# Kernel tuning notes

Measured on AMD Instinct MI355X. Metric: run time of the kernel, lower is better.

Reference implementation:

```python
import jax, jax.numpy as jnp
import numpy as np

T, S, B, H, NH, F = 256, 128, 32, 1024, 16, 4096
D = H // NH  # head dim


def setup_inputs() -> dict:
    key = jax.random.key(0)
    ks = jax.random.split(key, 14)
    w = lambda k, shape: jax.random.normal(k, shape, jnp.float32) * 0.02
    return {
        "x": jax.random.normal(ks[0], (T, B, H), jnp.float32),
        "src_bias": jnp.zeros((B, 1, 1, S), jnp.float32),
        "tgt_bias": jnp.zeros((B, 1, 1, T), jnp.float32),
        "memory": jax.random.normal(ks[1], (S, B, H), jnp.float32),
        # cross-attention projections
        "Wq": w(ks[2], (H, H)), "bq": jnp.zeros((H,), jnp.float32),
        "Wk": w(ks[3], (H, H)), "bk": jnp.zeros((H,), jnp.float32),
        "Wv": w(ks[4], (H, H)), "bv": jnp.zeros((H,), jnp.float32),
        "Wo": w(ks[5], (H, H)), "bo": jnp.zeros((H,), jnp.float32),
        # feed-forward
        "W1": w(ks[6], (H, F)), "b1": jnp.zeros((F,), jnp.float32),
        "W2": w(ks[7], (F, H)), "b2": jnp.zeros((H,), jnp.float32),
        # LSTM gates: input = cat(ffn_x, attn_ctx, h) -> 3H, output 4H (i,j,f,o)
        "Wg": w(ks[8], (3 * H, 4 * H)), "bg": jnp.zeros((4 * H,), jnp.float32),
    }


def _cross_attention(xq, mem, bias, Wq, bq, Wk, bk, Wv, bv, Wo, bo):
    # xq: [B,T,H], mem: [B,S,H], bias: [B,1,1,S]
    b, t, h = xq.shape
    q = (xq @ Wq + bq).reshape(b, t, NH, D) * (D ** -0.5)
    k = (mem @ Wk + bk).reshape(b, -1, NH, D)
    v = (mem @ Wv + bv).reshape(b, -1, NH, D)
    logits = jnp.einsum("bqhd,bkhd->bhqk", q, k) + bias
    wts = jax.nn.softmax(logits, axis=-1)
    ctx = jnp.einsum("bhqk,bkhd->bqhd", wts, v).reshape(b, t, h)
    return ctx @ Wo + bo


def reference(x, src_bias, tgt_bias, memory, Wq, bq, Wk, bk, Wv, bv, Wo, bo,
              W1, b1, W2, b2, Wg, bg):
    # cross attention (time-major -> batch-major -> time-major)
    c_attn = _cross_attention(jnp.transpose(x, (1, 0, 2)),
                              jnp.transpose(memory, (1, 0, 2)),
                              src_bias, Wq, bq, Wk, bk, Wv, bv, Wo, bo)
    c_attn = jnp.transpose(c_attn, (1, 0, 2))  # [T,B,H]

    # feed-forward on x (dropout disabled / eval mode)
    ffn_x = jax.nn.relu(x @ W1 + b1) @ W2 + b2  # [T,B,H]

    xs = jnp.concatenate([ffn_x, c_attn], axis=-1)  # [T,B,2H]
    c0 = jnp.zeros((x.shape[1], H), x.dtype)
    h0 = jnp.zeros((x.shape[1], H), x.dtype)

    def step(carry, xt):
        c, h = carry
        g = jnp.concatenate([xt, h], axis=-1) @ Wg + bg  # [B,4H]
        i = jax.nn.sigmoid(g[:, :H])
        j = jnp.tanh(g[:, H:2 * H])
        f = jax.nn.sigmoid(g[:, 2 * H:3 * H])
        o = jax.nn.sigmoid(g[:, 3 * H:])
        new_c = f * c + i * j
        new_h = o * new_c  # THUMT LSTMCell default activation=None
        return (new_c, new_h), new_h

    (c_f, h_f), hiddens = jax.lax.scan(step, (c0, h0), xs)
    return hiddens, c_f, h_f
```

## Files before the change

### kernel.cpp

```cpp
#include <hip/hip_runtime.h>
#include <cstdint>
#include <cstddef>

#define T_  256
#define S_  128
#define B_  32
#define H_  1024
#define NH_ 16
#define D_  64
#define F_  4096
#define TB_ (T_*B_)
#define SB_ (S_*B_)

typedef unsigned short u16;
typedef unsigned int   u32;
typedef unsigned long long u64;
typedef __attribute__((ext_vector_type(8))) short s16x8;
typedef __attribute__((ext_vector_type(4))) float f32x4;
typedef __attribute__((ext_vector_type(4))) u32  u32x4;

static __device__ __forceinline__ float b2f(u16 u) {
  union { u32 i; float f; } cv; cv.i = ((u32)u) << 16; return cv.f;
}
static __device__ __forceinline__ u16 f2b(float f) {
  union { float f; u32 i; } cv; cv.f = f;
  u32 u = cv.i;
  u32 r = (u + 0x7fffu + ((u >> 16) & 1u)) >> 16;
  return (u16)r;
}
static __device__ __forceinline__ float sigm(float x) {
  return 1.0f / (1.0f + __expf(-x));
}
static __device__ __forceinline__ float tanh_fast(float x) {
  float e2 = __expf(2.0f * x);
  return 1.0f - 2.0f / (e2 + 1.0f);
}

typedef const __attribute__((address_space(1))) void* gvoidp;
typedef __attribute__((address_space(3))) void* lvoidp;
static __device__ __forceinline__ void gl_lds16(const void* g, void* l) {
  __builtin_amdgcn_global_load_lds((gvoidp)g, (lvoidp)l, 16, 0, 0);
}

static __device__ __forceinline__ void cast_task(const float* __restrict__ in,
                                                 u16* __restrict__ out, int lb, int tid) {
  int i = lb * 256 + tid;
  float4 v = reinterpret_cast<const float4*>(in)[i];
  ushort4 o;
  o.x = f2b(v.x); o.y = f2b(v.y); o.z = f2b(v.z); o.w = f2b(v.w);
  reinterpret_cast<ushort4*>(out)[i] = o;
}

static __device__ __forceinline__ void tr32(const float* __restrict__ in,
                                            u16* __restrict__ out,
                                            int R, int C, int lin, int tid,
                                            float tile[32][33]) {
  const int gx = C >> 5;
  const int bx = lin % gx, by = lin / gx;
  const int c0 = bx << 5, r0 = by << 5;
  const int tx = tid & 31, ty = tid >> 5;
  #pragma unroll
  for (int k = 0; k < 32; k += 8)
    tile[ty + k][tx] = in[(size_t)(r0 + ty + k) * C + c0 + tx];
  __syncthreads();
  #pragma unroll
  for (int k = 0; k < 32; k += 8)
    out[(size_t)(c0 + ty + k) * R + r0 + tx] = f2b(tile[tx][ty + k]);
}

#define NB_SENT 1
#define NB_CX   8192
#define NB_CM   4096
#define NB_TSQ  1024
#define NB_TW1  4096
#define NB_TW2  4096
#define NB_TGX  8192
#define NB_TWH  4096
#define NB_PREP (NB_SENT + NB_CX + NB_CM + 4*NB_TSQ + NB_TW1 + NB_TW2 + NB_TGX + NB_TWH)

__global__ __launch_bounds__(256) void prep_all(
    const float* __restrict__ x, const float* __restrict__ mem,
    const float* __restrict__ Wq, const float* __restrict__ Wk,
    const float* __restrict__ Wv, const float* __restrict__ Wo,
    const float* __restrict__ W1, const float* __restrict__ W2,
    const float* __restrict__ Wg,
    u16* __restrict__ xb, u16* __restrict__ memb,
    u16* __restrict__ WqT, u16* __restrict__ WkT, u16* __restrict__ WvT,
    u16* __restrict__ WoT, u16* __restrict__ W1T, u16* __restrict__ W2T,
    u16* __restrict__ WgxT, u16* __restrict__ WhT, u32* __restrict__ sent)
{
  __shared__ float tile[32][33];
  int b = blockIdx.x;
  const int tid = threadIdx.x;
  if (b < NB_SENT) { sent[tid] = 0; sent[tid + 256] = 0; return; }
  b -= NB_SENT;
  if (b < NB_CX) { cast_task(x, xb, b, tid); return; }      b -= NB_CX;
  if (b < NB_CM) { cast_task(mem, memb, b, tid); return; }  b -= NB_CM;
  if (b < NB_TSQ) { tr32(Wq, WqT, H_, H_, b, tid, tile); return; }  b -= NB_TSQ;
  if (b < NB_TSQ) { tr32(Wk, WkT, H_, H_, b, tid, tile); return; }  b -= NB_TSQ;
  if (b < NB_TSQ) { tr32(Wv, WvT, H_, H_, b, tid, tile); return; }  b -= NB_TSQ;
  if (b < NB_TSQ) { tr32(Wo, WoT, H_, H_, b, tid, tile); return; }  b -= NB_TSQ;
  if (b < NB_TW1) { tr32(W1, W1T, H_, F_, b, tid, tile); return; }  b -= NB_TW1;
  if (b < NB_TW2) { tr32(W2, W2T, F_, H_, b, tid, tile); return; }  b -= NB_TW2;
  if (b < NB_TGX) { tr32(Wg, WgxT, 2 * H_, 4 * H_, b, tid, tile); return; } b -= NB_TGX;
  tr32(Wg + (size_t)(2 * H_) * (4 * H_), WhT, H_, 4 * H_, b, tid, tile);
}

static __device__ __forceinline__ void gemm_core(
    const u16* __restrict__ A, const u16* __restrict__ Bt,
    u16* __restrict__ Out, const float* __restrict__ bias,
    int Kdim, int ostride, float scale, int relu,
    int bx, int by, u16* As, u16* Bs)
{
  const int tid  = threadIdx.x;
  const int wave = tid >> 6, lane = tid & 63;
  const int quad = lane >> 4, l16 = lane & 15;
  const int bm = by << 7, bn = bx << 7;
  const int wm = (wave & 1) << 6, wn = (wave >> 1) << 6;
  f32x4 acc[4][4] = {};

  const int sr = wave * 32 + (lane >> 2);
  const int sc = (lane & 3) * 8;
  const u16* ga = &A [(size_t)(bm + sr) * Kdim + sc];
  const u16* gb = &Bt[(size_t)(bn + sr) * Kdim + sc];
  u16* lA = &As[wave * 1024];
  u16* lB = &Bs[wave * 1024];
  const size_t rowskip = (size_t)16 * Kdim;

  for (int k0 = 0; k0 < Kdim; k0 += 32) {
    gl_lds16(ga + k0,           lA);
    gl_lds16(ga + k0 + rowskip, lA + 512);
    gl_lds16(gb + k0,           lB);
    gl_lds16(gb + k0 + rowskip, lB + 512);
    __syncthreads();
    s16x8 af[4], bf[4];
    #pragma unroll
    for (int mt = 0; mt < 4; mt++)
      af[mt] = *(const s16x8*)&As[(wm + mt * 16 + l16) * 32 + quad * 8];
    #pragma unroll
    for (int nt = 0; nt < 4; nt++)
      bf[nt] = *(const s16x8*)&Bs[(wn + nt * 16 + l16) * 32 + quad * 8];
    #pragma unroll
    for (int mt = 0; mt < 4; mt++)
      #pragma unroll
      for (int nt = 0; nt < 4; nt++)
        acc[mt][nt] = __builtin_amdgcn_mfma_f32_16x16x32_bf16(af[mt], bf[nt], acc[mt][nt], 0, 0, 0);
    __syncthreads();
  }

  #pragma unroll
  for (int mt = 0; mt < 4; mt++) {
    #pragma unroll
    for (int nt = 0; nt < 4; nt++) {
      const int col = bn + wn + nt * 16 + l16;
      const float bv = bias[col];
      #pragma unroll
      for (int r = 0; r < 4; r++) {
        const int row = bm + wm + mt * 16 + quad * 4 + r;
        float vv = (acc[mt][nt][r] + bv) * scale;
        if (relu) vv = fmaxf(vv, 0.0f);
        Out[(size_t)row * ostride + col] = f2b(vv);
      }
    }
  }
}

struct GJob {
  const u16* A; const u16* Bt; u16* Out; const float* bias;
  int Kdim; int ostride; int relu; int gridx; int nblk; float scale;
};
struct GBatch { GJob j[4]; int starts[4]; int njobs; };

__global__ __launch_bounds__(256) void gemm_multi(GBatch gb)
{
  __shared__ __align__(16) u16 As[128 * 32];
  __shared__ __align__(16) u16 Bs[128 * 32];
  const int bid = blockIdx.x;
  int ji = 0;
  #pragma unroll
  for (int t = 1; t < 4; t++)
    if (t < gb.njobs && bid >= gb.starts[t]) ji = t;
  const GJob J = gb.j[ji];
  const int lin = bid - gb.starts[ji];
  const int wg = (lin & 7) * (J.nblk >> 3) + (lin >> 3);
  const int bx = wg % J.gridx, by = wg / J.gridx;
  gemm_core(J.A, J.Bt, J.Out, J.bias, J.Kdim, J.ostride, J.scale, J.relu, bx, by, As, Bs);
}

__global__ __launch_bounds__(256) void attn_kernel(
    const u16* __restrict__ q, const u16* __restrict__ k, const u16* __restrict__ v,
    const float* __restrict__ src_bias, u16* __restrict__ ctx)
{
  __shared__ u16 ks[S_ * D_];
  __shared__ u16 vs[S_ * D_];
  const int b  = blockIdx.x >> 4;
  const int nh = blockIdx.x & 15;
  const int tid = threadIdx.x;

  for (int i = tid; i < (S_ * D_) / 8; i += 256) {
    int s = i >> 3, c = (i & 7) * 8;
    *(uint4*)&ks[s * D_ + c] = *(const uint4*)&k[((size_t)(s * B_ + b)) * H_ + nh * D_ + c];
    *(uint4*)&vs[s * D_ + c] = *(const uint4*)&v[((size_t)(s * B_ + b)) * H_ + nh * D_ + c];
  }
  __syncthreads();

  const int t = tid;
  float qf[D_];
  const u16* qp = &q[((size_t)(t * B_ + b)) * H_ + nh * D_];
  #pragma unroll
  for (int c8 = 0; c8 < D_; c8 += 8) {
    uint4 qv = *(const uint4*)&qp[c8];
    const u16* pu = (const u16*)&qv;
    #pragma unroll
    for (int j = 0; j < 8; j++) qf[c8 + j] = b2f(pu[j]);
  }
  const float* bias = src_bias + b * S_;

  float m = -1e30f, l = 0.0f;
  for (int s = 0; s < S_; s++) {
    float dot = 0.0f;
    #pragma unroll
    for (int d = 0; d < D_; d++) dot += qf[d] * b2f(ks[s * D_ + d]);
    dot += bias[s];
    float nm = fmaxf(m, dot);
    l = l * __expf(m - nm) + __expf(dot - nm);
    m = nm;
  }
  float of[D_] = {};
  const float inv = 1.0f / l;
  for (int s = 0; s < S_; s++) {
    float dot = 0.0f;
    #pragma unroll
    for (int d = 0; d < D_; d++) dot += qf[d] * b2f(ks[s * D_ + d]);
    dot += bias[s];
    float w = __expf(dot - m) * inv;
    #pragma unroll
    for (int d = 0; d < D_; d++) of[d] += w * b2f(vs[s * D_ + d]);
  }
  u16* op = &ctx[((size_t)(t * B_ + b)) * H_ + nh * D_];
  #pragma unroll
  for (int c8 = 0; c8 < D_; c8 += 8) {
    u16 tmp[8];
    #pragma unroll
    for (int j = 0; j < 8; j++) tmp[j] = f2b(of[c8 + j]);
    *(uint4*)&op[c8] = *(const uint4*)tmp;
  }
}

#define ISSUE2(K) { \
  const u16* b0_ = hb + ((size_t)(wave * 16 + (K) * 2 + (quad >> 1))) * 512 + \
                   (quad & 1) * 8 + l16 * 16; \
  asm volatile("global_load_dwordx4 %0, %1, off sc0 sc1" : "=v"(ba[K][0]) : "v"(b0_) : "memory"); \
  asm volatile("global_load_dwordx4 %0, %1, off sc0 sc1" : "=v"(ba[K][1]) : "v"(b0_ + 256) : "memory"); }

#define DO_MFMA(A0,A1,KC)                                                           \
  { _Pragma("unroll") for (int g_ = 0; g_ < 3; g_++) {                              \
      s16x8 wf_ = *(const s16x8*)&Wl[wave][((g_ * 8 + (KC)) * 64 + lane) * 8];      \
      acc[g_][0] = __builtin_amdgcn_mfma_f32_16x16x32_bf16(A0, wf_, acc[g_][0], 0, 0, 0); \
      acc[g_][1] = __builtin_amdgcn_mfma_f32_16x16x32_bf16(A1, wf_, acc[g_][1], 0, 0, 0); } \
    acc[3][0] = __builtin_amdgcn_mfma_f32_16x16x32_bf16(A0, wo[KC], acc[3][0], 0, 0, 0);  \
    acc[3][1] = __builtin_amdgcn_mfma_f32_16x16x32_bf16(A1, wo[KC], acc[3][1], 0, 0, 0); }

#define CONSUME(K, NSTR) { \
  asm volatile("s_waitcnt vmcnt(" NSTR ")" ::: "memory"); \
  __builtin_amdgcn_sched_barrier(0); \
  DO_MFMA(ba[K][0], ba[K][1], K); }

__global__ __launch_bounds__(256, 1) void lstm_persistent(
    const u16* __restrict__ g_x, const u16* __restrict__ WhT,
    u16* __restrict__ hb16, u32* __restrict__ sent, float* __restrict__ out)
{
  __shared__ __align__(16) u16 Wl[4][3 * 8 * 64 * 8];
  __shared__ float P[4][4][32][17];
  const int bk = blockIdx.x, tid = threadIdx.x;
  const int wave = tid >> 6, lane = tid & 63;
  const int quad = lane >> 4, l16 = lane & 15;

  for (int i = lane; i < 3 * 8 * 64; i += 64) {
    const int g  = (i >> 9) & 3;
    const int kc = (i >> 6) & 7;
    const int row = g * H_ + bk * 16 + (lane & 15);
    const int col = wave * 256 + kc * 32 + (lane >> 4) * 8;
    *(uint4*)&Wl[wave][i * 8] = *(const uint4*)&WhT[(size_t)row * H_ + col];
  }
  s16x8 wo[8];
  {
    const int row = 3 * H_ + bk * 16 + (lane & 15);
    const int colb = wave * 256 + (lane >> 4) * 8;
    #pragma unroll
    for (int kc = 0; kc < 8; kc++)
      wo[kc] = *(const s16x8*)&WhT[(size_t)row * H_ + colb + kc * 32];
  }
  __syncthreads();

  const int pb = tid >> 4, pc = tid & 15;
  const int col = bk * 16 + pc;
  float creg[2] = {0.0f, 0.0f};

  float gxp[2][4];
  #pragma unroll
  for (int ii = 0; ii < 2; ii++)
    #pragma unroll
    for (int g = 0; g < 4; g++)
      gxp[ii][g] = b2f(g_x[((size_t)(pb + ii * 16)) * (4 * H_) + g * H_ + col]);

  s16x8 ba[8][2];

  for (int t = 0; t < T_; t++) {
    if (t > 0) {
      const u32 st = (u32)t;
      const u16* hb = hb16 + ((t & 1) ^ 1) * 32768;

      { const u32* sp = sent + ((size_t)(((t & 1) ^ 1) * 256 + wave * 64 + lane));
        u32 sv;
        do {
          asm volatile("global_load_dword %0, %1, off sc0 sc1\n\ts_waitcnt vmcnt(0)"
                       : "=v"(sv) : "v"(sp) : "memory");
        } while (!__all(sv == st)); }

      f32x4 acc[4][2] = {};
      ISSUE2(0) ISSUE2(1) ISSUE2(2) ISSUE2(3)
      ISSUE2(4) ISSUE2(5) ISSUE2(6) ISSUE2(7)
      CONSUME(0, "14") CONSUME(1, "12") CONSUME(2, "10") CONSUME(3, "8")
      CONSUME(4, "6")  CONSUME(5, "4")  CONSUME(6, "2")  CONSUME(7, "0")

      #pragma unroll
      for (int g = 0; g < 4; g++)
        #pragma unroll
        for (int mt = 0; mt < 2; mt++)
          #pragma unroll
          for (int r = 0; r < 4; r++)
            P[wave][g][mt * 16 + quad * 4 + r][l16] = acc[g][mt][r];
    }
    __syncthreads();

    float gs[2][4];
    #pragma unroll
    for (int ii = 0; ii < 2; ii++) {
      const int b_ = pb + ii * 16;
      #pragma unroll
      for (int g = 0; g < 4; g++) {
        float s = gxp[ii][g];
        if (t > 0) s += P[0][g][b_][pc] + P[1][g][b_][pc] + P[2][g][b_][pc] + P[3][g][b_][pc];
        gs[ii][g] = s;
      }
    }
    __syncthreads();

    float hn[2], cn[2];
    #pragma unroll
    for (int ii = 0; ii < 2; ii++) {
      const float iv = sigm(gs[ii][0]);
      const float jv = tanh_fast(gs[ii][1]);
      const float fv = sigm(gs[ii][2]);
      const float ov = sigm(gs[ii][3]);
      cn[ii] = fv * creg[ii] + iv * jv;
      hn[ii] = ov * cn[ii];
      creg[ii] = cn[ii];
    }

    {
      u32 lo0 = f2b(hn[0]), lo1 = f2b(hn[1]);
      u32 hi0 = __shfl_down(lo0, 1), hi1 = __shfl_down(lo1, 1);
      if ((pc & 1) == 0) {
        u32* hw32 = (u32*)(hb16 + (t & 1) * 32768);
        u32 dw0 = lo0 | (hi0 << 16);
        u32 dw1 = lo1 | (hi1 << 16);
        __hip_atomic_store(&hw32[(size_t)bk * 256 + pb * 8 + (pc >> 1)], dw0,
                           __ATOMIC_RELAXED, __HIP_MEMORY_SCOPE_AGENT);
        __hip_atomic_store(&hw32[(size_t)bk * 256 + (pb + 16) * 8 + (pc >> 1)], dw1,
                           __ATOMIC_RELAXED, __HIP_MEMORY_SCOPE_AGENT);
      }
      asm volatile("s_waitcnt vmcnt(0)" ::: "memory");
      if (lane == 0)
        __hip_atomic_store(&sent[(size_t)(t & 1) * 256 + bk * 4 + wave], (u32)(t + 1),
                           __ATOMIC_RELAXED, __HIP_MEMORY_SCOPE_AGENT);
    }

    #pragma unroll
    for (int ii = 0; ii < 2; ii++) {
      const int b_ = pb + ii * 16;
      out[(size_t)t * (B_ * H_) + b_ * H_ + col] = hn[ii];
      if (t == T_ - 1) {
        out[(size_t)T_ * B_ * H_ + b_ * H_ + col] = cn[ii];
        out[(size_t)T_ * B_ * H_ + B_ * H_ + b_ * H_ + col] = hn[ii];
      }
    }
    if (t < T_ - 1) {
      #pragma unroll
      for (int ii = 0; ii < 2; ii++)
        #pragma unroll
        for (int g = 0; g < 4; g++)
          gxp[ii][g] = b2f(g_x[((size_t)(t + 1) * B_ + pb + ii * 16) * (4 * H_) + g * H_ + col]);
    }
  }
}

extern "C" void kernel_launch(void* const* d_in, const int* in_sizes, int n_in,
                              void* d_out, int out_size, void* d_ws, size_t ws_size,
                              hipStream_t stream)
{
  const float* x        = (const float*)d_in[0];
  const float* src_bias = (const float*)d_in[1];
  const float* mem      = (const float*)d_in[3];
  const float* Wq = (const float*)d_in[4];  const float* bq = (const float*)d_in[5];
  const float* Wk = (const float*)d_in[6];  const float* bk = (const float*)d_in[7];
  const float* Wv = (const float*)d_in[8];  const float* bv = (const float*)d_in[9];
  const float* Wo = (const float*)d_in[10]; const float* bo = (const float*)d_in[11];
  const float* W1 = (const float*)d_in[12]; const float* b1f = (const float*)d_in[13];
  const float* W2 = (const float*)d_in[14]; const float* b2f_ = (const float*)d_in[15];
  const float* Wg = (const float*)d_in[16]; const float* bg = (const float*)d_in[17];
  float* out = (float*)d_out;

  char* p = (char*)d_ws;
  u16* xb   = (u16*)p; p += (size_t)TB_ * H_ * 2;
  u16* memb = (u16*)p; p += (size_t)SB_ * H_ * 2;
  u16* WqT  = (u16*)p; p += (size_t)H_ * H_ * 2;
  u16* WkT  = (u16*)p; p += (size_t)H_ * H_ * 2;
  u16* WvT  = (u16*)p; p += (size_t)H_ * H_ * 2;
  u16* WoT  = (u16*)p; p += (size_t)H_ * H_ * 2;
  u16* W1T  = (u16*)p; p += (size_t)F_ * H_ * 2;
  u16* W2T  = (u16*)p; p += (size_t)H_ * F_ * 2;
  u16* WgxT = (u16*)p; p += (size_t)(4 * H_) * (2 * H_) * 2;
  u16* WhT  = (u16*)p; p += (size_t)(4 * H_) * H_ * 2;
  u16* qb   = (u16*)p; p += (size_t)TB_ * H_ * 2;
  u16* kb   = (u16*)p; p += (size_t)SB_ * H_ * 2;
  u16* vb   = (u16*)p; p += (size_t)SB_ * H_ * 2;
  u16* ctxb = (u16*)p; p += (size_t)TB_ * H_ * 2;
  u16* xs   = (u16*)p; p += (size_t)TB_ * (2 * H_) * 2;
  u16* h1   = (u16*)p; p += (size_t)TB_ * F_ * 2;
  u16* hb16 = (u16*)p; p += (size_t)2 * 32768 * 2;
  u32* sent = (u32*)p; p += (size_t)2 * 256 * 4;
  u16* gx   = h1;

  prep_all<<<dim3(NB_PREP), dim3(256), 0, stream>>>(
      x, mem, Wq, Wk, Wv, Wo, W1, W2, Wg,
      xb, memb, WqT, WkT, WvT, WoT, W1T, W2T, WgxT, WhT, sent);

  GBatch gb1 = {};
  gb1.j[0] = { xb,   WqT, qb, bq,  H_,     H_,     0,  H_ / 128,     TB_ / 128 * (H_ / 128),      0.125f };
  gb1.j[1] = { memb, WkT, kb, bk,  H_,     H_,     0,  H_ / 128,     SB_ / 128 * (H_ / 128),      1.0f   };
  gb1.j[2] = { memb, WvT, vb, bv,  H_,     H_,     0,  H_ / 128,     SB_ / 128 * (H_ / 128),      1.0f   };
  gb1.j[3] = { xb,   W1T, h1, b1f, H_,     F_,     1,  F_ / 128,     TB_ / 128 * (F_ / 128),      1.0f   };
  gb1.starts[0] = 0;
  gb1.starts[1] = gb1.j[0].nblk;
  gb1.starts[2] = gb1.starts[1] + gb1.j[1].nblk;
  gb1.starts[3] = gb1.starts[2] + gb1.j[2].nblk;
  gb1.njobs = 4;
  const int nb1 = gb1.starts[3] + gb1.j[3].nblk;
  gemm_multi<<<dim3(nb1), dim3(256), 0, stream>>>(gb1);

  attn_kernel<<<dim3(B_ * NH_), dim3(256), 0, stream>>>(qb, kb, vb, src_bias, ctxb);

  GBatch gb2 = {};
  gb2.j[0] = { ctxb, WoT, xs + H_, bo,   H_, 2 * H_, 0, H_ / 128, TB_ / 128 * (H_ / 128), 1.0f };
  gb2.j[1] = { h1,   W2T, xs,      b2f_, F_, 2 * H_, 0, H_ / 128, TB_ / 128 * (H_ / 128), 1.0f };
  gb2.starts[0] = 0;
  gb2.starts[1] = gb2.j[0].nblk;
  gb2.njobs = 2;
  const int nb2 = gb2.starts[1] + gb2.j[1].nblk;
  gemm_multi<<<dim3(nb2), dim3(256), 0, stream>>>(gb2);

  GBatch gb3 = {};
  gb3.j[0] = { xs, WgxT, gx, bg, 2 * H_, 4 * H_, 0, 4 * H_ / 128, TB_ / 128 * (4 * H_ / 128), 1.0f };
  gb3.starts[0] = 0;
  gb3.njobs = 1;
  gemm_multi<<<dim3(gb3.j[0].nblk), dim3(256), 0, stream>>>(gb3);

  lstm_persistent<<<dim3(64), dim3(256), 0, stream>>>(gx, WhT, hb16, sent, out);
}
```

Before: 1.697 ms.

## Replace 128x128 GEMM with double-buffered 256x256 tile pipelined kernel

Replaces the 128x128-tile, 4-wave, single-buffered GEMM with a 256x256-tile, 8-wave kernel. It stages the next K-tile into a second LDS buffer while MFMAs run, using manual vmcnt waits, s_barrier and setprio, and XOR-swizzles LDS rows to avoid bank conflicts. The larger tiles raise data reuse per block and the overlap hides global load latency. The cost is fewer blocks per GEMM, which can under-fill the GPU for the small K/V projections, plus 128KB of LDS per block and heavier register use.

```diff
diff --git a/kernel.cpp b/kernel.cpp
--- a/kernel.cpp
+++ b/kernel.cpp
@@ -106,64 +106,9 @@
   tr32(Wg + (size_t)(2 * H_) * (4 * H_), WhT, H_, 4 * H_, b, tid, tile);
 }
 
-static __device__ __forceinline__ void gemm_core(
-    const u16* __restrict__ A, const u16* __restrict__ Bt,
-    u16* __restrict__ Out, const float* __restrict__ bias,
-    int Kdim, int ostride, float scale, int relu,
-    int bx, int by, u16* As, u16* Bs)
-{
-  const int tid  = threadIdx.x;
-  const int wave = tid >> 6, lane = tid & 63;
-  const int quad = lane >> 4, l16 = lane & 15;
-  const int bm = by << 7, bn = bx << 7;
-  const int wm = (wave & 1) << 6, wn = (wave >> 1) << 6;
-  f32x4 acc[4][4] = {};
-
-  const int sr = wave * 32 + (lane >> 2);
-  const int sc = (lane & 3) * 8;
-  const u16* ga = &A [(size_t)(bm + sr) * Kdim + sc];
-  const u16* gb = &Bt[(size_t)(bn + sr) * Kdim + sc];
-  u16* lA = &As[wave * 1024];
-  u16* lB = &Bs[wave * 1024];
-  const size_t rowskip = (size_t)16 * Kdim;
-
-  for (int k0 = 0; k0 < Kdim; k0 += 32) {
-    gl_lds16(ga + k0,           lA);
-    gl_lds16(ga + k0 + rowskip, lA + 512);
-    gl_lds16(gb + k0,           lB);
-    gl_lds16(gb + k0 + rowskip, lB + 512);
-    __syncthreads();
-    s16x8 af[4], bf[4];
-    #pragma unroll
-    for (int mt = 0; mt < 4; mt++)
-      af[mt] = *(const s16x8*)&As[(wm + mt * 16 + l16) * 32 + quad * 8];
-    #pragma unroll
-    for (int nt = 0; nt < 4; nt++)
-      bf[nt] = *(const s16x8*)&Bs[(wn + nt * 16 + l16) * 32 + quad * 8];
-    #pragma unroll
-    for (int mt = 0; mt < 4; mt++)
-      #pragma unroll
-      for (int nt = 0; nt < 4; nt++)
-        acc[mt][nt] = __builtin_amdgcn_mfma_f32_16x16x32_bf16(af[mt], bf[nt], acc[mt][nt], 0, 0, 0);
-    __syncthreads();
-  }
-
-  #pragma unroll
-  for (int mt = 0; mt < 4; mt++) {
-    #pragma unroll
-    for (int nt = 0; nt < 4; nt++) {
-      const int col = bn + wn + nt * 16 + l16;
-      const float bv = bias[col];
-      #pragma unroll
-      for (int r = 0; r < 4; r++) {
-        const int row = bm + wm + mt * 16 + quad * 4 + r;
-        float vv = (acc[mt][nt][r] + bv) * scale;
-        if (relu) vv = fmaxf(vv, 0.0f);
-        Out[(size_t)row * ostride + col] = f2b(vv);
-      }
-    }
-  }
-}
+#define SBAR      asm volatile("s_barrier" ::: "memory")
+#define VMCNT4    asm volatile("s_waitcnt vmcnt(4)" ::: "memory")
+#define VMCNT0    asm volatile("s_waitcnt vmcnt(0)" ::: "memory")
 
 struct GJob {
   const u16* A; const u16* Bt; u16* Out; const float* bias;
@@ -171,10 +116,25 @@
 };
 struct GBatch { GJob j[4]; int starts[4]; int njobs; };
 
-__global__ __launch_bounds__(256) void gemm_multi(GBatch gb)
+static __device__ __forceinline__ void stage_region(
+    const u16* __restrict__ src, int Kdim, int row0,
+    int kt, int kh, char* lds_region, int tid) {
+  const int w  = tid >> 6;
+  const int r  = tid >> 2;
+  const int cs = (tid & 3) ^ ((tid >> 3) & 3);
+  const int kbase = kt * 64 + kh * 32 + cs * 8;
+  gl_lds16(src + (size_t)(row0 + r) * Kdim + kbase,        lds_region + w * 1024);
+  gl_lds16(src + (size_t)(row0 + 128 + r) * Kdim + kbase,  lds_region + 8192 + w * 1024);
+}
+
+static __device__ __forceinline__ s16x8 ldsf(const char* sm, int base, int row, int quad) {
+  return *(const s16x8*)(sm + base + row * 64 + ((quad ^ ((row >> 1) & 3)) << 4));
+}
+
+__global__ __launch_bounds__(512, 2) void gemm256(GBatch gb)
 {
-  __shared__ __align__(16) u16 As[128 * 32];
-  __shared__ __align__(16) u16 Bs[128 * 32];
+  __shared__ __align__(16) u16 smem[65536];
+  char* sm = (char*)smem;
   const int bid = blockIdx.x;
   int ji = 0;
   #pragma unroll
@@ -184,7 +144,109 @@
   const int lin = bid - gb.starts[ji];
   const int wg = (lin & 7) * (J.nblk >> 3) + (lin >> 3);
   const int bx = wg % J.gridx, by = wg / J.gridx;
-  gemm_core(J.A, J.Bt, J.Out, J.bias, J.Kdim, J.ostride, J.scale, J.relu, bx, by, As, Bs);
+  const int bm = by << 8, bn = bx << 8;
+
+  const int tid = threadIdx.x;
+  const int wavei = tid >> 6, lane = tid & 63;
+  const int quad = lane >> 4, l16 = lane & 15;
+  const int wm = wavei >> 2, wn = wavei & 3;
+  const int NT = J.Kdim >> 6;
+  const int arow = wm * 128;
+  const int brow = wn * 64;
+
+  f32x4 acc[8][4] = {};
+
+  stage_region(J.A,  J.Kdim, bm, 0, 0, sm + 0,     tid);
+  stage_region(J.Bt, J.Kdim, bn, 0, 0, sm + 32768, tid);
+  stage_region(J.A,  J.Kdim, bm, 0, 1, sm + 16384, tid);
+  stage_region(J.Bt, J.Kdim, bn, 0, 1, sm + 49152, tid);
+  VMCNT4;
+  SBAR;
+
+  for (int kt = 0; kt < NT; kt++) {
+    const int p = (kt & 1) << 16;
+    const int q = p ^ 65536;
+    const int Ab = p, Bb = p + 32768;
+    const bool st = (kt + 1 < NT);
+    s16x8 af[8], b0, b1;
+
+    #pragma unroll
+    for (int mi = 0; mi < 8; mi++)
+      af[mi] = ldsf(sm, Ab, arow + mi * 16 + l16, quad);
+    b0 = ldsf(sm, Bb, brow + l16, quad);
+    b1 = ldsf(sm, Bb, brow + 16 + l16, quad);
+    if (st) stage_region(J.A, J.Kdim, bm, kt + 1, 0, sm + q, tid);
+    SBAR;
+    __builtin_amdgcn_s_setprio(1);
+    #pragma unroll
+    for (int mi = 0; mi < 8; mi++) {
+      acc[mi][0] = __builtin_amdgcn_mfma_f32_16x16x32_bf16(af[mi], b0, acc[mi][0], 0, 0, 0);
+      acc[mi][1] = __builtin_amdgcn_mfma_f32_16x16x32_bf16(af[mi], b1, acc[mi][1], 0, 0, 0);
+    }
+    __builtin_amdgcn_s_setprio(0);
+    SBAR;
+
+    b0 = ldsf(sm, Bb, brow + 32 + l16, quad);
+    b1 = ldsf(sm, Bb, brow + 48 + l16, quad);
+    if (st) stage_region(J.Bt, J.Kdim, bn, kt + 1, 0, sm + q + 32768, tid);
+    SBAR;
+    __builtin_amdgcn_s_setprio(1);
+    #pragma unroll
+    for (int mi = 0; mi < 8; mi++) {
+      acc[mi][2] = __builtin_amdgcn_mfma_f32_16x16x32_bf16(af[mi], b0, acc[mi][2], 0, 0, 0);
+      acc[mi][3] = __builtin_amdgcn_mfma_f32_16x16x32_bf16(af[mi], b1, acc[mi][3], 0, 0, 0);
+    }
+    __builtin_amdgcn_s_setprio(0);
+    if (st) { VMCNT4; } else { VMCNT0; }
+    SBAR;
+
+    const int Ab1 = Ab + 16384, Bb1 = Bb + 16384;
+    #pragma unroll
+    for (int mi = 0; mi < 8; mi++)
+      af[mi] = ldsf(sm, Ab1, arow + mi * 16 + l16, quad);
+    b0 = ldsf(sm, Bb1, brow + l16, quad);
+    b1 = ldsf(sm, Bb1, brow + 16 + l16, quad);
+    if (st) stage_region(J.A, J.Kdim, bm, kt + 1, 1, sm + q + 16384, tid);
+    SBAR;
+    __builtin_amdgcn_s_setprio(1);
+    #pragma unroll
+    for (int mi = 0; mi < 8; mi++) {
+      acc[mi][0] = __builtin_amdgcn_mfma_f32_16x16x32_bf16(af[mi], b0, acc[mi][0], 0, 0, 0);
+      acc[mi][1] = __builtin_amdgcn_mfma_f32_16x16x32_bf16(af[mi], b1, acc[mi][1], 0, 0, 0);
+    }
+    __builtin_amdgcn_s_setprio(0);
+    SBAR;
+
+    b0 = ldsf(sm, Bb1, brow + 32 + l16, quad);
+    b1 = ldsf(sm, Bb1, brow + 48 + l16, quad);
+    if (st) stage_region(J.Bt, J.Kdim, bn, kt + 1, 1, sm + q + 49152, tid);
+    SBAR;
+    __builtin_amdgcn_s_setprio(1);
+    #pragma unroll
+    for (int mi = 0; mi < 8; mi++) {
+      acc[mi][2] = __builtin_amdgcn_mfma_f32_16x16x32_bf16(af[mi], b0, acc[mi][2], 0, 0, 0);
+      acc[mi][3] = __builtin_amdgcn_mfma_f32_16x16x32_bf16(af[mi], b1, acc[mi][3], 0, 0, 0);
+    }
+    __builtin_amdgcn_s_setprio(0);
+    if (st) { VMCNT4; }
+    SBAR;
+  }
+
+  #pragma unroll
+  for (int mi = 0; mi < 8; mi++) {
+    #pragma unroll
+    for (int nj = 0; nj < 4; nj++) {
+      const int colo = bn + wn * 64 + nj * 16 + l16;
+      const float bv = J.bias[colo];
+      #pragma unroll
+      for (int r = 0; r < 4; r++) {
+        const int rowo = bm + wm * 128 + mi * 16 + quad * 4 + r;
+        float vv = (acc[mi][nj][r] + bv) * J.scale;
+        if (J.relu) vv = fmaxf(vv, 0.0f);
+        J.Out[(size_t)rowo * J.ostride + colo] = f2b(vv);
+      }
+    }
+  }
 }
 
 __global__ __launch_bounds__(256) void attn_kernel(
@@ -438,34 +500,34 @@
       xb, memb, WqT, WkT, WvT, WoT, W1T, W2T, WgxT, WhT, sent);
 
   GBatch gb1 = {};
-  gb1.j[0] = { xb,   WqT, qb, bq,  H_,     H_,     0,  H_ / 128,     TB_ / 128 * (H_ / 128),      0.125f };
-  gb1.j[1] = { memb, WkT, kb, bk,  H_,     H_,     0,  H_ / 128,     SB_ / 128 * (H_ / 128),      1.0f   };
-  gb1.j[2] = { memb, WvT, vb, bv,  H_,     H_,     0,  H_ / 128,     SB_ / 128 * (H_ / 128),      1.0f   };
-  gb1.j[3] = { xb,   W1T, h1, b1f, H_,     F_,     1,  F_ / 128,     TB_ / 128 * (F_ / 128),      1.0f   };
+  gb1.j[0] = { xb,   WqT, qb, bq,  H_, H_, 0, H_ / 256, (TB_ / 256) * (H_ / 256), 0.125f };
+  gb1.j[1] = { memb, WkT, kb, bk,  H_, H_, 0, H_ / 256, (SB_ / 256) * (H_ / 256), 1.0f   };
+  gb1.j[2] = { memb, WvT, vb, bv,  H_, H_, 0, H_ / 256, (SB_ / 256) * (H_ / 256), 1.0f   };
+  gb1.j[3] = { xb,   W1T, h1, b1f, H_, F_, 1, F_ / 256, (TB_ / 256) * (F_ / 256), 1.0f   };
   gb1.starts[0] = 0;
   gb1.starts[1] = gb1.j[0].nblk;
   gb1.starts[2] = gb1.starts[1] + gb1.j[1].nblk;
   gb1.starts[3] = gb1.starts[2] + gb1.j[2].nblk;
   gb1.njobs = 4;
   const int nb1 = gb1.starts[3] + gb1.j[3].nblk;
-  gemm_multi<<<dim3(nb1), dim3(256), 0, stream>>>(gb1);
+  gemm256<<<dim3(nb1), dim3(512), 0, stream>>>(gb1);
 
   attn_kernel<<<dim3(B_ * NH_), dim3(256), 0, stream>>>(qb, kb, vb, src_bias, ctxb);
 
   GBatch gb2 = {};
-  gb2.j[0] = { ctxb, WoT, xs + H_, bo,   H_, 2 * H_, 0, H_ / 128, TB_ / 128 * (H_ / 128), 1.0f };
-  gb2.j[1] = { h1,   W2T, xs,      b2f_, F_, 2 * H_, 0, H_ / 128, TB_ / 128 * (H_ / 128), 1.0f };
+  gb2.j[0] = { ctxb, WoT, xs + H_, bo,   H_, 2 * H_, 0, H_ / 256, (TB_ / 256) * (H_ / 256), 1.0f };
+  gb2.j[1] = { h1,   W2T, xs,      b2f_, F_, 2 * H_, 0, H_ / 256, (TB_ / 256) * (H_ / 256), 1.0f };
   gb2.starts[0] = 0;
   gb2.starts[1] = gb2.j[0].nblk;
   gb2.njobs = 2;
   const int nb2 = gb2.starts[1] + gb2.j[1].nblk;
-  gemm_multi<<<dim3(nb2), dim3(256), 0, stream>>>(gb2);
+  gemm256<<<dim3(nb2), dim3(512), 0, stream>>>(gb2);
 
   GBatch gb3 = {};
-  gb3.j[0] = { xs, WgxT, gx, bg, 2 * H_, 4 * H_, 0, 4 * H_ / 128, TB_ / 128 * (4 * H_ / 128), 1.0f };
+  gb3.j[0] = { xs, WgxT, gx, bg, 2 * H_, 4 * H_, 0, 4 * H_ / 256, (TB_ / 256) * (4 * H_ / 256), 1.0f };
   gb3.starts[0] = 0;
   gb3.njobs = 1;
-  gemm_multi<<<dim3(gb3.j[0].nblk), dim3(256), 0, stream>>>(gb3);
+  gemm256<<<dim3(gb3.j[0].nblk), dim3(512), 0, stream>>>(gb3);
 
   lstm_persistent<<<dim3(64), dim3(256), 0, stream>>>(gx, WhT, hb16, sent, out);
 }
```

Measured after the change: 1.591 ms (median of 2 runs). 6.2% less time.
